# Performance work log

Hardware: AMD Instinct MI355X
Metric: run time of the kernel (lower is better)

Reference implementation:

```python
import jax, jax.numpy as jnp
import numpy as np
from jax import lax

OUTH, OUTW = 7, 7
SCALE = 0.0625  # 1/16


def setup_inputs() -> dict:
    key = jax.random.key(0)
    k1, k2, k3, k4, k5, k6 = jax.random.split(key, 6)
    B, C, H, W = 1, 512, 50, 50
    N = 1024
    x = jax.random.normal(k1, (B, C, H, W), dtype=jnp.float32)
    bidx = jax.random.randint(k2, (N,), 0, B).astype(jnp.float32)
    x1 = jax.random.uniform(k3, (N,), minval=0.0, maxval=600.0)
    y1 = jax.random.uniform(k4, (N,), minval=0.0, maxval=600.0)
    bw = jax.random.uniform(k5, (N,), minval=16.0, maxval=220.0)
    bh = jax.random.uniform(k6, (N,), minval=16.0, maxval=220.0)
    x2 = jnp.clip(x1 + bw, 0.0, 799.0)
    y2 = jnp.clip(y1 + bh, 0.0, 799.0)
    rois = jnp.stack([bidx, x1, y1, x2, y2], axis=1)  # [N,5]
    return {"x": x, "rois": rois}


def _roi_max_pool(x, rois, outh, outw, scale):
    B, C, H, W = x.shape
    N = rois.shape[0]
    b = rois[:, 0].astype(jnp.int32)
    ws = jnp.round(rois[:, 1] * scale).astype(jnp.int32)
    hs = jnp.round(rois[:, 2] * scale).astype(jnp.int32)
    we = jnp.round(rois[:, 3] * scale).astype(jnp.int32)
    he = jnp.round(rois[:, 4] * scale).astype(jnp.int32)
    # malformed ROIs forced to 1x1 (matches kernel)
    roi_w = jnp.maximum(we - ws + 1, 1).astype(jnp.float32)
    roi_h = jnp.maximum(he - hs + 1, 1).astype(jnp.float32)
    bin_h = roi_h / outh
    bin_w = roi_w / outw
    ph = jnp.arange(outh, dtype=jnp.float32)
    pw = jnp.arange(outw, dtype=jnp.float32)
    hstart = jnp.clip(jnp.floor(bin_h[:, None] * ph).astype(jnp.int32) + hs[:, None], 0, H)   # [N,outh]
    hend = jnp.clip(jnp.ceil(bin_h[:, None] * (ph + 1.0)).astype(jnp.int32) + hs[:, None], 0, H)
    wstart = jnp.clip(jnp.floor(bin_w[:, None] * pw).astype(jnp.int32) + ws[:, None], 0, W)   # [N,outw]
    wend = jnp.clip(jnp.ceil(bin_w[:, None] * (pw + 1.0)).astype(jnp.int32) + ws[:, None], 0, W)

    # max window extent of one bin (static)
    Kh = int(np.ceil((H + 1) / outh)) + 2
    Kw = int(np.ceil((W + 1) / outw)) + 2
    dh, dw = np.meshgrid(np.arange(Kh), np.arange(Kw), indexing="ij")  # row-major like kernel
    offs = jnp.asarray(np.stack([dh.ravel(), dw.ravel()], axis=1), dtype=jnp.int32)  # [Kh*Kw,2]

    x_ng = lax.stop_gradient(x)
    bv0 = jnp.full((N, outh, outw, C), -jnp.inf, dtype=x.dtype)
    bi0 = jnp.full((N, outh, outw, C), -1, dtype=jnp.int32)

    def step(carry, d):
        bv, bi = carry
        h = hstart + d[0]                      # [N,outh]
        w = wstart + d[1]                      # [N,outw]
        vh = h < hend
        vw = w < wend
        hc = jnp.clip(h, 0, H - 1)
        wc = jnp.clip(w, 0, W - 1)
        # gather window values -> [N,outh,outw,C]
        vals = x_ng[b[:, None, None], :, hc[:, :, None], wc[:, None, :]]
        valid = (vh[:, :, None] & vw[:, None, :])[..., None]
        lin = (hc[:, :, None] * W + wc[:, None, :])[..., None]
        upd = valid & (vals > bv)              # strict '>' -> first-argmax like kernel
        bv = jnp.where(upd, vals, bv)
        bi = jnp.where(upd, lin, bi)
        return (bv, bi), None

    (_, bi), _ = lax.scan(step, (bv0, bi0), offs)
    bi = lax.stop_gradient(bi)

    # differentiable gather of the max values via argmax indices
    xf = x.reshape(B, C, H * W)
    cc = jnp.arange(C)[None, None, None, :]
    gathered = xf[b[:, None, None, None], cc, jnp.maximum(bi, 0)]  # [N,outh,outw,C]
    out = jnp.where(bi >= 0, gathered, jnp.zeros((), x.dtype))      # empty bins -> 0
    return out.transpose(0, 3, 1, 2)  # [N,C,outh,outw]


def reference(x, rois):
    return _roi_max_pool(x, rois, OUTH, OUTW, SCALE)
```

## Files before the change

### kernel.cpp

```cpp
#include <hip/hip_runtime.h>


#define HH 50
#define WW 50
#define CC 512
#define OH 7
#define OW 7
#define NBINS 49
#define HW (HH * WW)
#define CG 64

__device__ __forceinline__ int4 compute_bounds(const float* __restrict__ r,
                                               int ph, int pw) {
    const float RCP7 = 1.0f / 7.0f;
    int ws = (int)rintf(r[1] * 0.0625f);
    int hs = (int)rintf(r[2] * 0.0625f);
    int we = (int)rintf(r[3] * 0.0625f);
    int he = (int)rintf(r[4] * 0.0625f);
    float roi_w = (float)max(we - ws + 1, 1);
    float roi_h = (float)max(he - hs + 1, 1);
    float bin_h = roi_h * RCP7;
    float bin_w = roi_w * RCP7;
    int hstart = min(max((int)floorf(bin_h * (float)ph) + hs, 0), HH);
    int hend   = min(max((int)ceilf (bin_h * (float)(ph + 1)) + hs, 0), HH);
    int wstart = min(max((int)floorf(bin_w * (float)pw) + ws, 0), WW);
    int wend   = min(max((int)ceilf (bin_w * (float)(pw + 1)) + ws, 0), WW);
    return make_int4(hstart, hend, wstart, wend);
}

__global__ __launch_bounds__(256) void transpose_x(const float* __restrict__ x,
                                                   float* __restrict__ xt) {
    __shared__ float tile[64][65];
    int tx = threadIdx.x & 63;
    int tg = threadIdx.x >> 6;
    int hw0 = blockIdx.x * 64;
    int c0  = blockIdx.y * 64;
    #pragma unroll
    for (int i = 0; i < 16; ++i) {
        int r  = tg * 16 + i;
        int hw = hw0 + tx;
        if (hw < HW) tile[r][tx] = x[(size_t)(c0 + r) * HW + hw];
    }
    __syncthreads();
    #pragma unroll
    for (int i = 0; i < 16; ++i) {
        int r  = tg * 16 + i;
        int hw = hw0 + r;
        if (hw < HW) xt[(size_t)hw * CC + c0 + tx] = tile[tx][r];
    }
}

__global__ __launch_bounds__(256) void roi_pool_t(const float* __restrict__ xt,
                                                  const float* __restrict__ rois,
                                                  float* __restrict__ out) {
    __shared__ int4  sbnd[NBINS];
    __shared__ float stile[CG * NBINS];
    int tid = threadIdx.x;
    int n   = blockIdx.x >> 3;
    int cg  = blockIdx.x & 7;

    const float* r = rois + (size_t)n * 5;
    if (tid < NBINS) sbnd[tid] = compute_bounds(r, tid / OW, tid % OW);
    __syncthreads();

    int lane = tid & 63;
    int wv   = tid >> 6;
    const float* base = xt + cg * CG + lane;

    for (int bin = wv; bin < NBINS; bin += 4) {
        int4 bd = sbnd[bin];
        int h0 = __builtin_amdgcn_readfirstlane(bd.x);
        int h1 = __builtin_amdgcn_readfirstlane(bd.y);
        int w0 = __builtin_amdgcn_readfirstlane(bd.z);
        int w1 = __builtin_amdgcn_readfirstlane(bd.w);
        float m = -INFINITY;
        for (int h = h0; h < h1; ++h)
            for (int w = w0; w < w1; ++w)
                m = fmaxf(m, base[(size_t)(h * WW + w) * CC]);
        bool ne = (h0 < h1) && (w0 < w1);
        stile[lane * NBINS + bin] = ne ? m : 0.0f;
    }
    __syncthreads();

    size_t ob4 = (((size_t)n * CC + cg * CG) * NBINS) >> 2;
    float4* o4 = (float4*)out;
    const float4* s4 = (const float4*)stile;
    for (int t = tid; t < (CG * NBINS) / 4; t += 256)
        o4[ob4 + t] = s4[t];
}

__global__ __launch_bounds__(256) void roi_pool_fused(const float* __restrict__ x,
                                                      const float* __restrict__ rois,
                                                      float* __restrict__ out,
                                                      int total) {
    int idx = blockIdx.x * blockDim.x + threadIdx.x;
    if (idx >= total) return;
    int pw = idx % OW;
    int t  = idx / OW;
    int ph = t % OH;
    t /= OH;
    int c = t % CC;
    int n = t / CC;
    const float* r = rois + (size_t)n * 5;
    int4 bnd = compute_bounds(r, ph, pw);
    int b = (int)r[0];
    const float* plane = x + ((size_t)b * CC + c) * HW;
    float m = -INFINITY;
    for (int h = bnd.x; h < bnd.y; ++h) {
        const float* row = plane + h * WW;
        for (int w = bnd.z; w < bnd.w; ++w)
            m = fmaxf(m, row[w]);
    }
    bool nonempty = (bnd.x < bnd.y) && (bnd.z < bnd.w);
    out[idx] = nonempty ? m : 0.0f;
}

extern "C" void kernel_launch(void* const* d_in, const int* in_sizes, int n_in,
                              void* d_out, int out_size, void* d_ws, size_t ws_size,
                              hipStream_t stream) {
    const float* x    = (const float*)d_in[0];
    const float* rois = (const float*)d_in[1];
    float* out = (float*)d_out;
    int nrois = in_sizes[1] / 5;

    size_t need = (size_t)HW * CC * sizeof(float);
    if (ws_size >= need) {
        float* xt = (float*)d_ws;
        transpose_x<<<dim3((HW + 63) / 64, CC / 64), 256, 0, stream>>>(x, xt);
        roi_pool_t<<<nrois * (CC / CG), 256, 0, stream>>>(xt, rois, out);
    } else {
        roi_pool_fused<<<(out_size + 255) / 256, 256, 0, stream>>>(x, rois, out,
                                                                   out_size);
    }
}
```

Baseline: 167.8 us.

## Process ROI pooling by bin row with float2 channel pairs per lane

```diff
diff --git a/kernel.cpp b/kernel.cpp
--- a/kernel.cpp
+++ b/kernel.cpp
@@ -8,24 +8,25 @@
 #define OW 7
 #define NBINS 49
 #define HW (HH * WW)
-#define CG 64
+#define CG 128
+
+__device__ __forceinline__ int2 dim_bounds(float lo_px, float hi_px, int p,
+                                           int limit) {
+    const float RCP7 = 1.0f / 7.0f;
+    int s = (int)rintf(lo_px * 0.0625f);
+    int e = (int)rintf(hi_px * 0.0625f);
+    float span = (float)max(e - s + 1, 1);
+    float bin  = span * RCP7;
+    int b0 = min(max((int)floorf(bin * (float)p) + s, 0), limit);
+    int b1 = min(max((int)ceilf (bin * (float)(p + 1)) + s, 0), limit);
+    return make_int2(b0, b1);
+}
 
 __device__ __forceinline__ int4 compute_bounds(const float* __restrict__ r,
                                                int ph, int pw) {
-    const float RCP7 = 1.0f / 7.0f;
-    int ws = (int)rintf(r[1] * 0.0625f);
-    int hs = (int)rintf(r[2] * 0.0625f);
-    int we = (int)rintf(r[3] * 0.0625f);
-    int he = (int)rintf(r[4] * 0.0625f);
-    float roi_w = (float)max(we - ws + 1, 1);
-    float roi_h = (float)max(he - hs + 1, 1);
-    float bin_h = roi_h * RCP7;
-    float bin_w = roi_w * RCP7;
-    int hstart = min(max((int)floorf(bin_h * (float)ph) + hs, 0), HH);
-    int hend   = min(max((int)ceilf (bin_h * (float)(ph + 1)) + hs, 0), HH);
-    int wstart = min(max((int)floorf(bin_w * (float)pw) + ws, 0), WW);
-    int wend   = min(max((int)ceilf (bin_w * (float)(pw + 1)) + ws, 0), WW);
-    return make_int4(hstart, hend, wstart, wend);
+    int2 hb = dim_bounds(r[2], r[4], ph, HH);
+    int2 wb = dim_bounds(r[1], r[3], pw, WW);
+    return make_int4(hb.x, hb.y, wb.x, wb.y);
 }
 
 __global__ __launch_bounds__(256) void transpose_x(const float* __restrict__ x,
@@ -50,35 +51,59 @@
     }
 }
 
-__global__ __launch_bounds__(256) void roi_pool_t(const float* __restrict__ xt,
-                                                  const float* __restrict__ rois,
-                                                  float* __restrict__ out) {
-    __shared__ int4  sbnd[NBINS];
+__global__ __launch_bounds__(256) void roi_pool_cells(
+    const float* __restrict__ xt, const float* __restrict__ rois,
+    float* __restrict__ out)
+{
+    __shared__ int2  shb[OH], swb[OW];
     __shared__ float stile[CG * NBINS];
     int tid = threadIdx.x;
-    int n   = blockIdx.x >> 3;
-    int cg  = blockIdx.x & 7;
+    int n   = blockIdx.x >> 2;
+    int cg  = blockIdx.x & 3;
 
     const float* r = rois + (size_t)n * 5;
-    if (tid < NBINS) sbnd[tid] = compute_bounds(r, tid / OW, tid % OW);
+    if (tid < OH)                         shb[tid]     = dim_bounds(r[2], r[4], tid, HH);
+    else if (tid >= 8 && tid < 8 + OW)    swb[tid - 8] = dim_bounds(r[1], r[3], tid - 8, WW);
     __syncthreads();
 
     int lane = tid & 63;
     int wv   = tid >> 6;
-    const float* base = xt + cg * CG + lane;
+    const float* base = xt + cg * CG + lane * 2;
 
-    for (int bin = wv; bin < NBINS; bin += 4) {
-        int4 bd = sbnd[bin];
-        int h0 = __builtin_amdgcn_readfirstlane(bd.x);
-        int h1 = __builtin_amdgcn_readfirstlane(bd.y);
-        int w0 = __builtin_amdgcn_readfirstlane(bd.z);
-        int w1 = __builtin_amdgcn_readfirstlane(bd.w);
-        float m = -INFINITY;
-        for (int h = h0; h < h1; ++h)
-            for (int w = w0; w < w1; ++w)
-                m = fmaxf(m, base[(size_t)(h * WW + w) * CC]);
-        bool ne = (h0 < h1) && (w0 < w1);
-        stile[lane * NBINS + bin] = ne ? m : 0.0f;
+    for (int phi = 0; phi < 2; ++phi) {
+        int ph = wv + phi * 4;
+        if (ph >= OH) break;
+        int2 hb = shb[ph];
+        int h0 = __builtin_amdgcn_readfirstlane(hb.x);
+        int h1 = __builtin_amdgcn_readfirstlane(hb.y);
+
+        float2 acc[OW];
+        #pragma unroll
+        for (int pw = 0; pw < OW; ++pw) { acc[pw].x = -INFINITY; acc[pw].y = -INFINITY; }
+
+        #pragma unroll
+        for (int pw = 0; pw < OW; ++pw) {
+            int2 wb = swb[pw];
+            int w0 = __builtin_amdgcn_readfirstlane(wb.x);
+            int w1 = __builtin_amdgcn_readfirstlane(wb.y);
+            for (int h = h0; h < h1; ++h) {
+                const float* rowp = base + (size_t)(h * WW) * CC;
+                for (int w = w0; w < w1; ++w) {
+                    float2 v = *(const float2*)&rowp[(size_t)w * CC];
+                    acc[pw].x = fmaxf(acc[pw].x, v.x);
+                    acc[pw].y = fmaxf(acc[pw].y, v.y);
+                }
+            }
+        }
+
+        #pragma unroll
+        for (int pw = 0; pw < OW; ++pw) {
+            int2 wb = swb[pw];
+            bool ne = (h0 < h1) && (wb.x < wb.y);
+            int bin = ph * OW + pw;
+            stile[(lane * 2 + 0) * NBINS + bin] = ne ? acc[pw].x : 0.0f;
+            stile[(lane * 2 + 1) * NBINS + bin] = ne ? acc[pw].y : 0.0f;
+        }
     }
     __syncthreads();
 
@@ -127,7 +152,7 @@
     if (ws_size >= need) {
         float* xt = (float*)d_ws;
         transpose_x<<<dim3((HW + 63) / 64, CC / 64), 256, 0, stream>>>(x, xt);
-        roi_pool_t<<<nrois * (CC / CG), 256, 0, stream>>>(xt, rois, out);
+        roi_pool_cells<<<nrois * (CC / CG), 256, 0, stream>>>(xt, rois, out);
     } else {
         roi_pool_fused<<<(out_size + 255) / 256, 256, 0, stream>>>(x, rois, out,
                                                                    out_size);
```

Measured after the change: 151.1 us. 1.11x faster.
